# Kernel optimization log

Measured on AMD Instinct MI355X. Metric: run time of the kernel, lower is better.

The kernel has to match this reference:

```python
import jax, jax.numpy as jnp
import numpy as np

W = 2  # config.spatial_width in NeuTraj


def _offsets():
    d = np.arange(-W, W + 1)
    dx, dy = np.meshgrid(d, d, indexing='ij')
    return jnp.asarray(np.stack([dx.ravel(), dy.ravel()], axis=1))  # [(2W+1)^2, 2]


def setup_inputs() -> dict:
    key = jax.random.key(0)
    ks = jax.random.split(key, 10)
    B, H, F = 8192, 128, 128
    G = 1100
    N = G + 3 * W  # 1106
    stdv = 1.0 / np.sqrt(H)
    u = lambda k, s: jax.random.uniform(k, s, jnp.float32, -stdv, stdv)
    return {
        'input_feat': jax.random.normal(ks[0], (B, F), jnp.float32),
        'hx': jax.random.normal(ks[1], (B, H), jnp.float32),
        'grid_idx': jax.random.randint(ks[2], (B, 2), 0, G),
        'memory': jax.random.normal(ks[3], (N, N, H), jnp.float32) * 0.1,
        'w_ih': u(ks[4], (4 * H, F)),
        'w_hh': u(ks[5], (4 * H, H)),
        'b_ih': u(ks[6], (4 * H,)),
        'b_hh': u(ks[7], (4 * H,)),
        'w_out': u(ks[8], (H, 2 * H)),  # Attention.linear_out
        'b_out': u(ks[9], (H,)),
    }


def reference(input_feat, hx, grid_idx, memory, w_ih, w_hh, b_ih, b_hh, w_out, b_out):
    g = grid_idx + W  # shift by spatial_width, as in the torch code
    # GRU-style gate GEMMs (4 gates: reset, update, new, spatial)
    gi = input_feat @ w_ih.T + b_ih
    gh = hx @ w_hh.T + b_hh
    i_r, i_i, i_n, i_s = jnp.split(gi, 4, axis=1)
    h_r, h_i, h_n, h_s = jnp.split(gh, 4, axis=1)
    resetgate = jax.nn.sigmoid(i_r + h_r)
    updategate = jax.nn.sigmoid(i_i + h_i)
    spatialgate = jax.nn.sigmoid(i_s + h_s)
    newgate = jnp.tanh(i_n + resetgate * h_n)

    # cy_hh = newgate.data  -> detached attention query
    q = jax.lax.stop_gradient(newgate)

    # gather (2W+1)^2 = 25 neighboring grid cells per sample: cs [B, 25, H]
    nb = g[:, None, :] + _offsets()[None]  # [B, 25, 2]
    cs = memory[nb[..., 0], nb[..., 1]]

    # Luong attention: scores -> softmax -> mix -> concat -> linear -> tanh
    scores = jnp.einsum('bh,blh->bl', q, cs)
    attn = jax.nn.softmax(scores, axis=1)
    mix = jnp.einsum('bl,blh->bh', attn, cs)
    combined = jnp.concatenate([mix, q], axis=1)  # [B, 2H]
    atten_cs = jnp.tanh(combined @ w_out.T + b_out)

    curr_state = newgate + spatialgate * atten_cs
    hyy = curr_state + updategate * (hx - curr_state)

    # incell scatter write-back (all .data in torch -> stop_gradient)
    sg = jax.lax.stop_gradient(spatialgate)
    cd = jax.lax.stop_gradient(hyy)
    gx, gy = g[:, 0], g[:, 1]
    updates = sg * memory[gx, gy] + (1.0 - sg) * cd
    new_memory = memory.at[gx, gy].set(jax.lax.stop_gradient(updates))
    return hyy, new_memory
```

## Files before the change

### kernel.cpp

```cpp
#include <hip/hip_runtime.h>
#include <hip/hip_bf16.h>

typedef float f32x4 __attribute__((ext_vector_type(4)));

#define B_  8192
#define H_  128
#define NW  1106
#define NC  640
#define KK  256

static const size_t N4TOT = (size_t)NW * NW * H_ / 4;

#define SL1 6000000UL
#define SL2 4000000UL

#define K1_CPB 1024
#define K2_CB  2048
#define K2_CPB 1024
#define K3_CPB 2048

__device__ __forceinline__ float sigmf(float x) { return 1.0f / (1.0f + expf(-x)); }

__device__ __forceinline__ void copy_span(const f32x4* __restrict__ src,
                                          f32x4* __restrict__ dst,
                                          size_t lo, size_t hi,
                                          size_t ctid, size_t cthreads) {
    for (size_t i = lo + ctid; i < hi; i += cthreads) {
        f32x4 v = __builtin_nontemporal_load(src + i);
        __builtin_nontemporal_store(v, dst + i);
    }
}

__global__ __launch_bounds__(256) void k1_gates(
    const float* __restrict__ xf, const float* __restrict__ hx,
    const float* __restrict__ w_ih, const float* __restrict__ w_hh,
    float* __restrict__ Cbuf, const int* __restrict__ gidx, int* __restrict__ winner,
    const f32x4* __restrict__ src, f32x4* __restrict__ dst, size_t lo, size_t hi) {
    __shared__ float As[64][36];
    __shared__ float Ws[32][132];
    int bid = blockIdx.x, tid = threadIdx.x;
    if (bid >= 640) {
        int rel = bid - 640;
        if (rel < 32) {
            int b = rel * 256 + tid;
            int gx = gidx[2 * b] + 2, gy = gidx[2 * b + 1] + 2;
            atomicMax(&winner[gx * NW + gy], b);
        }
        size_t ctid = (size_t)rel * 256 + tid;
        copy_span(src, dst, lo, hi, ctid, (size_t)(gridDim.x - 640) * 256);
        return;
    }
    int bx = bid & 127;
    int strip = bid >> 7;
    size_t m0 = (size_t)bx * 64;
    int n0 = strip * 128;
    int wbase = (strip == 0) ? 0 : (strip == 1) ? 128 : (strip == 2) ? 384 : 256;
    int kstart = (strip == 4) ? 128 : 0;
    int kend   = (strip == 3) ? 128 : 256;

    int tn = tid & 15, tm = tid >> 4;
    float acc[4][8];
#pragma unroll
    for (int i = 0; i < 4; ++i)
#pragma unroll
        for (int j = 0; j < 8; ++j) acc[i][j] = 0.0f;

    for (int k0 = kstart; k0 < kend; k0 += 32) {
        const float* asrc = (k0 < 128) ? xf : hx;
        const float* wsrc = (strip == 3) ? w_ih
                          : (strip == 4) ? w_hh
                          : (k0 < 128 ? w_ih : w_hh);
        int koff = k0 & 127;
        __syncthreads();
#pragma unroll
        for (int p = 0; p < 2; ++p) {
            int f = tid + 256 * p; int r = f >> 3, cq = f & 7;
            float4 v = *(const float4*)(asrc + (m0 + r) * 128 + koff + 4 * cq);
            *(float4*)(&As[r][4 * cq]) = v;
        }
#pragma unroll
        for (int p = 0; p < 4; ++p) {
            int f = tid + 256 * p; int c = f >> 3, cq = f & 7;
            float4 v = *(const float4*)(wsrc + (size_t)(wbase + c) * 128 + koff + 4 * cq);
            Ws[4 * cq + 0][c] = v.x; Ws[4 * cq + 1][c] = v.y;
            Ws[4 * cq + 2][c] = v.z; Ws[4 * cq + 3][c] = v.w;
        }
        __syncthreads();
#pragma unroll
        for (int kk = 0; kk < 32; ++kk) {
            float4 w0 = *(const float4*)(&Ws[kk][4 * tn]);
            float4 w1 = *(const float4*)(&Ws[kk][64 + 4 * tn]);
#pragma unroll
            for (int i = 0; i < 4; ++i) {
                float a = As[4 * tm + i][kk];
                acc[i][0] += a * w0.x; acc[i][1] += a * w0.y;
                acc[i][2] += a * w0.z; acc[i][3] += a * w0.w;
                acc[i][4] += a * w1.x; acc[i][5] += a * w1.y;
                acc[i][6] += a * w1.z; acc[i][7] += a * w1.w;
            }
        }
    }
#pragma unroll
    for (int i = 0; i < 4; ++i) {
        size_t row = m0 + 4 * tm + i;
        float4 v0 = make_float4(acc[i][0], acc[i][1], acc[i][2], acc[i][3]);
        float4 v1 = make_float4(acc[i][4], acc[i][5], acc[i][6], acc[i][7]);
        *(float4*)(Cbuf + row * NC + n0 + 4 * tn) = v0;
        *(float4*)(Cbuf + row * NC + n0 + 64 + 4 * tn) = v1;
    }
}

__global__ __launch_bounds__(256) void k2_attn(
    const float* __restrict__ C, const float* __restrict__ memory,
    const int* __restrict__ gidx, const float* __restrict__ b_ih,
    const float* __restrict__ b_hh, float* __restrict__ mixq,
    float* __restrict__ ug, float* __restrict__ sg,
    const f32x4* __restrict__ src, f32x4* __restrict__ dst, size_t lo, size_t hi) {
    int bid = blockIdx.x, tid = threadIdx.x;
    if (bid >= K2_CB) {
        size_t ctid = (size_t)(bid - K2_CB) * 256 + tid;
        copy_span(src, dst, lo, hi, ctid, (size_t)(gridDim.x - K2_CB) * 256);
        return;
    }
    int b = bid * 4 + (tid >> 6);
    int t = tid & 63;
    int t1 = t + 64;
    const float* Crow = C + (size_t)b * NC;
    float r0 = sigmf(Crow[t]        + b_ih[t]        + b_hh[t]);
    float r1 = sigmf(Crow[t1]       + b_ih[t1]       + b_hh[t1]);
    float u0 = sigmf(Crow[128 + t]  + b_ih[128 + t]  + b_hh[128 + t]);
    float u1 = sigmf(Crow[128 + t1] + b_ih[128 + t1] + b_hh[128 + t1]);
    float s0 = sigmf(Crow[256 + t]  + b_ih[384 + t]  + b_hh[384 + t]);
    float s1 = sigmf(Crow[256 + t1] + b_ih[384 + t1] + b_hh[384 + t1]);
    float n0 = tanhf(Crow[384 + t]  + b_ih[256 + t]  + r0 * (Crow[512 + t]  + b_hh[256 + t]));
    float n1 = tanhf(Crow[384 + t1] + b_ih[256 + t1] + r1 * (Crow[512 + t1] + b_hh[256 + t1]));

    int gx = gidx[2 * b] + 2, gy = gidx[2 * b + 1] + 2;
    const float* base = memory + ((size_t)gx * NW + gy) * H_ + t;
    float cs0[25], cs1[25];
#pragma unroll
    for (int l = 0; l < 25; ++l) {
        int dx = l / 5 - 2, dy = l % 5 - 2;
        const float* row = base + ((long)dx * NW + dy) * H_;
        cs0[l] = row[0];
        cs1[l] = row[64];
    }
    float sc[25];
#pragma unroll
    for (int l = 0; l < 25; ++l) {
        float p = n0 * cs0[l] + n1 * cs1[l];
#pragma unroll
        for (int w = 1; w < 64; w <<= 1) p += __shfl_xor(p, w, 64);
        sc[l] = p;
    }
    float mx = sc[0];
#pragma unroll
    for (int l = 1; l < 25; ++l) mx = fmaxf(mx, sc[l]);
    float den = 0.0f, mix0 = 0.0f, mix1 = 0.0f;
#pragma unroll
    for (int l = 0; l < 25; ++l) {
        float e = expf(sc[l] - mx);
        den += e;
        mix0 += e * cs0[l];
        mix1 += e * cs1[l];
    }
    float inv = 1.0f / den;
    mix0 *= inv; mix1 *= inv;

    float* mq = mixq + (size_t)b * 256;
    mq[t] = mix0; mq[t1] = mix1; mq[128 + t] = n0; mq[128 + t1] = n1;
    ug[(size_t)b * H_ + t] = u0; ug[(size_t)b * H_ + t1] = u1;
    sg[(size_t)b * H_ + t] = s0; sg[(size_t)b * H_ + t1] = s1;
}

__global__ __launch_bounds__(256) void k3_final(
    const float* __restrict__ mixq, const float* __restrict__ w_out,
    const float* __restrict__ b_out, const float* __restrict__ sg,
    const float* __restrict__ ug, const float* __restrict__ hx,
    const float* __restrict__ memory, const int* __restrict__ gidx,
    const int* __restrict__ winner, float* __restrict__ hyy,
    float* __restrict__ newmem,
    const f32x4* __restrict__ src, f32x4* __restrict__ dst, size_t lo, size_t hi) {
    __shared__ float As[64][36];
    __shared__ float Ws[32][132];
    int bid = blockIdx.x, tid = threadIdx.x;
    if (bid >= 128) {
        size_t ctid = (size_t)(bid - 128) * 256 + tid;
        size_t nthr = (size_t)(gridDim.x - 128) * 256;
        for (size_t i = lo + ctid; i < hi; i += nthr) {
            if (winner[i >> 5] < 0) {
                f32x4 v = __builtin_nontemporal_load(src + i);
                __builtin_nontemporal_store(v, dst + i);
            }
        }
        return;
    }
    size_t m0 = (size_t)bid * 64;
    int tn = tid & 15, tm = tid >> 4;
    float acc[4][8];
#pragma unroll
    for (int i = 0; i < 4; ++i)
#pragma unroll
        for (int j = 0; j < 8; ++j) acc[i][j] = 0.0f;

    for (int k0 = 0; k0 < KK; k0 += 32) {
        __syncthreads();
#pragma unroll
        for (int p = 0; p < 2; ++p) {
            int f = tid + 256 * p; int r = f >> 3, cq = f & 7;
            float4 v = *(const float4*)(mixq + (m0 + r) * KK + k0 + 4 * cq);
            *(float4*)(&As[r][4 * cq]) = v;
        }
#pragma unroll
        for (int p = 0; p < 4; ++p) {
            int f = tid + 256 * p; int c = f >> 3, cq = f & 7;
            float4 v = *(const float4*)(w_out + (size_t)c * KK + k0 + 4 * cq);
            Ws[4 * cq + 0][c] = v.x; Ws[4 * cq + 1][c] = v.y;
            Ws[4 * cq + 2][c] = v.z; Ws[4 * cq + 3][c] = v.w;
        }
        __syncthreads();
#pragma unroll
        for (int kk = 0; kk < 32; ++kk) {
            float4 w0 = *(const float4*)(&Ws[kk][4 * tn]);
            float4 w1 = *(const float4*)(&Ws[kk][64 + 4 * tn]);
#pragma unroll
            for (int i = 0; i < 4; ++i) {
                float a = As[4 * tm + i][kk];
                acc[i][0] += a * w0.x; acc[i][1] += a * w0.y;
                acc[i][2] += a * w0.z; acc[i][3] += a * w0.w;
                acc[i][4] += a * w1.x; acc[i][5] += a * w1.y;
                acc[i][6] += a * w1.z; acc[i][7] += a * w1.w;
            }
        }
    }
#pragma unroll
    for (int i = 0; i < 4; ++i) {
        size_t row = m0 + 4 * tm + i;
        int gx = gidx[2 * row] + 2, gy = gidx[2 * row + 1] + 2;
        size_t cell = (size_t)gx * NW + gy;
        bool win = (winner[cell] == (int)row);
#pragma unroll
        for (int half = 0; half < 2; ++half) {
#pragma unroll
            for (int j = 0; j < 4; ++j) {
                int col = half * 64 + 4 * tn + j;
                float a = acc[i][half * 4 + j];
                float atten = tanhf(a + b_out[col]);
                float s = sg[row * H_ + col];
                float u = ug[row * H_ + col];
                float q = mixq[row * 256 + 128 + col];
                float curr = q + s * atten;
                float hy = curr + u * (hx[row * H_ + col] - curr);
                hyy[row * H_ + col] = hy;
                if (win) {
                    float m = memory[cell * H_ + col];
                    newmem[cell * H_ + col] = s * m + (1.0f - s) * hy;
                }
            }
        }
    }
}

__global__ void copy_kernel(const f32x4* __restrict__ src, f32x4* __restrict__ dst, size_t n4) {
    size_t stride = (size_t)gridDim.x * blockDim.x;
    for (size_t i = (size_t)blockIdx.x * blockDim.x + threadIdx.x; i < n4; i += stride) {
        f32x4 v = __builtin_nontemporal_load(src + i);
        __builtin_nontemporal_store(v, dst + i);
    }
}

extern "C" void kernel_launch(void* const* d_in, const int* in_sizes, int n_in,
                              void* d_out, int out_size, void* d_ws, size_t ws_size,
                              hipStream_t stream) {
    const float* xf     = (const float*)d_in[0];
    const float* hx     = (const float*)d_in[1];
    const int*   gidx   = (const int*)d_in[2];
    const float* memory = (const float*)d_in[3];
    const float* w_ih   = (const float*)d_in[4];
    const float* w_hh   = (const float*)d_in[5];
    const float* b_ih   = (const float*)d_in[6];
    const float* b_hh   = (const float*)d_in[7];
    const float* w_out  = (const float*)d_in[8];
    const float* b_out  = (const float*)d_in[9];

    float* out    = (float*)d_out;
    float* hyy    = out;
    float* newmem = out + (size_t)B_ * H_;
    const f32x4* src4 = (const f32x4*)memory;
    f32x4*       dst4 = (f32x4*)newmem;

    float* wsf    = (float*)d_ws;
    float* mixq   = wsf;
    float* ug     = mixq + (size_t)B_ * 256;
    float* sg     = ug + (size_t)B_ * H_;
    int*   winner = (int*)(sg + (size_t)B_ * H_);
    char*  pers_end = (char*)(winner + (size_t)NW * NW);
    size_t pers_bytes = (size_t)(pers_end - (char*)d_ws);

    size_t CF = (size_t)B_ * NC;
    bool distributed = (ws_size >= pers_bytes + CF * sizeof(float));
    float* Cbuf = distributed ? (float*)pers_end : newmem;

    hipMemsetAsync(winner, 0xFF, (size_t)NW * NW * sizeof(int), stream);

    if (distributed) {
        size_t a1 = SL1, b1 = a1 + SL2;
        k1_gates<<<640 + K1_CPB, 256, 0, stream>>>(
            xf, hx, w_ih, w_hh, Cbuf, gidx, winner, src4, dst4, 0, a1);
        k2_attn<<<K2_CB + K2_CPB, 256, 0, stream>>>(
            Cbuf, memory, gidx, b_ih, b_hh, mixq, ug, sg, src4, dst4, a1, b1);
        k3_final<<<128 + K3_CPB, 256, 0, stream>>>(
            mixq, w_out, b_out, sg, ug, hx, memory, gidx, winner, hyy, newmem,
            src4, dst4, b1, N4TOT);
    } else {
        k1_gates<<<640 + 32, 256, 0, stream>>>(
            xf, hx, w_ih, w_hh, Cbuf, gidx, winner, src4, dst4, 0, 0);
        k2_attn<<<K2_CB, 256, 0, stream>>>(
            Cbuf, memory, gidx, b_ih, b_hh, mixq, ug, sg, src4, dst4, 0, 0);
        copy_kernel<<<2048, 256, 0, stream>>>(src4, dst4, N4TOT);
        k3_final<<<128 + 32, 256, 0, stream>>>(
            mixq, w_out, b_out, sg, ug, hx, memory, gidx, winner, hyy, newmem,
            src4, dst4, 0, 0);
    }
}
```

Baseline: 333.5 us.

## Replace memset with copy-carrying init kernel and rebalance memory copy across stages

Replaces the hipMemsetAsync of the winner table with a k0_init kernel that both fills winner with -1 and copies the first slice of memory into the output. The copy slices for k1, k2 and k3 are rebalanced so more of the bulk copy overlaps with the compute kernels. k2_attn now uses one 64-thread block per sample instead of four samples per 256-thread block, which adds more copy blocks. The aim is to hide more of the memory copy behind compute and to drop the separate memset launch, at the risk of less efficient scheduling with small blocks.

Result: faster. 319.1 us (-4.3%).

```diff
diff --git a/kernel.cpp b/kernel.cpp
--- a/kernel.cpp
+++ b/kernel.cpp
@@ -11,13 +11,14 @@
 
 static const size_t N4TOT = (size_t)NW * NW * H_ / 4;
 
-#define SL1 6000000UL
-#define SL2 4000000UL
-
-#define K1_CPB 1024
-#define K2_CB  2048
-#define K2_CPB 1024
-#define K3_CPB 2048
+#define S0_ 4000000UL
+#define S1_ 10000000UL
+#define S2_ 14500000UL
+
+#define K0_BLKS 1024
+#define K1_CPB  1024
+#define K2_CPB  4096
+#define K3_CPB  2048
 
 __device__ __forceinline__ float sigmf(float x) { return 1.0f / (1.0f + expf(-x)); }
 
@@ -29,6 +30,15 @@
         f32x4 v = __builtin_nontemporal_load(src + i);
         __builtin_nontemporal_store(v, dst + i);
     }
+}
+
+__global__ __launch_bounds__(256) void k0_init(
+    int* __restrict__ winner,
+    const f32x4* __restrict__ src, f32x4* __restrict__ dst, size_t lo, size_t hi) {
+    size_t gt = (size_t)blockIdx.x * 256 + threadIdx.x;
+    size_t nthr = (size_t)gridDim.x * 256;
+    for (size_t i = gt; i < (size_t)NW * NW; i += nthr) winner[i] = -1;
+    copy_span(src, dst, lo, hi, gt, nthr);
 }
 
 __global__ __launch_bounds__(256) void k1_gates(
@@ -110,20 +120,20 @@
     }
 }
 
-__global__ __launch_bounds__(256) void k2_attn(
+__global__ __launch_bounds__(64) void k2_attn(
     const float* __restrict__ C, const float* __restrict__ memory,
     const int* __restrict__ gidx, const float* __restrict__ b_ih,
     const float* __restrict__ b_hh, float* __restrict__ mixq,
     float* __restrict__ ug, float* __restrict__ sg,
     const f32x4* __restrict__ src, f32x4* __restrict__ dst, size_t lo, size_t hi) {
-    int bid = blockIdx.x, tid = threadIdx.x;
-    if (bid >= K2_CB) {
-        size_t ctid = (size_t)(bid - K2_CB) * 256 + tid;
-        copy_span(src, dst, lo, hi, ctid, (size_t)(gridDim.x - K2_CB) * 256);
+    int bid = blockIdx.x;
+    int t = threadIdx.x;
+    if (bid >= B_) {
+        size_t ctid = (size_t)(bid - B_) * 64 + t;
+        copy_span(src, dst, lo, hi, ctid, (size_t)(gridDim.x - B_) * 64);
         return;
     }
-    int b = bid * 4 + (tid >> 6);
-    int t = tid & 63;
+    int b = bid;
     int t1 = t + 64;
     const float* Crow = C + (size_t)b * NC;
     float r0 = sigmf(Crow[t]        + b_ih[t]        + b_hh[t]);
@@ -301,21 +311,20 @@
     bool distributed = (ws_size >= pers_bytes + CF * sizeof(float));
     float* Cbuf = distributed ? (float*)pers_end : newmem;
 
-    hipMemsetAsync(winner, 0xFF, (size_t)NW * NW * sizeof(int), stream);
-
     if (distributed) {
-        size_t a1 = SL1, b1 = a1 + SL2;
+        k0_init<<<K0_BLKS, 256, 0, stream>>>(winner, src4, dst4, 0, S0_);
         k1_gates<<<640 + K1_CPB, 256, 0, stream>>>(
-            xf, hx, w_ih, w_hh, Cbuf, gidx, winner, src4, dst4, 0, a1);
-        k2_attn<<<K2_CB + K2_CPB, 256, 0, stream>>>(
-            Cbuf, memory, gidx, b_ih, b_hh, mixq, ug, sg, src4, dst4, a1, b1);
+            xf, hx, w_ih, w_hh, Cbuf, gidx, winner, src4, dst4, S0_, S1_);
+        k2_attn<<<B_ + K2_CPB, 64, 0, stream>>>(
+            Cbuf, memory, gidx, b_ih, b_hh, mixq, ug, sg, src4, dst4, S1_, S2_);
         k3_final<<<128 + K3_CPB, 256, 0, stream>>>(
             mixq, w_out, b_out, sg, ug, hx, memory, gidx, winner, hyy, newmem,
-            src4, dst4, b1, N4TOT);
+            src4, dst4, S2_, N4TOT);
     } else {
+        k0_init<<<K0_BLKS, 256, 0, stream>>>(winner, src4, dst4, 0, 0);
         k1_gates<<<640 + 32, 256, 0, stream>>>(
             xf, hx, w_ih, w_hh, Cbuf, gidx, winner, src4, dst4, 0, 0);
-        k2_attn<<<K2_CB, 256, 0, stream>>>(
+        k2_attn<<<B_, 64, 0, stream>>>(
             Cbuf, memory, gidx, b_ih, b_hh, mixq, ug, sg, src4, dst4, 0, 0);
         copy_kernel<<<2048, 256, 0, stream>>>(src4, dst4, N4TOT);
         k3_final<<<128 + 32, 256, 0, stream>>>(
```
